# Kernel optimization log

Measured on AMD Instinct MI355X. Metric: run time of the kernel, lower is better.

The kernel has to match this reference:

```python
import jax, jax.numpy as jnp
import numpy as np

WEIGHT_BITS = 4           # weight_bit_width for both convs
SCALE_MIN = 2e-16         # scaling_min_val from CommonIntWeightPerTensorQuant


def fake_quant_per_channel(w, bits):
    """Brevitas-style per-output-channel symmetric narrow-range int fake quant.
    scale = max|w| over each output channel / (2^(bits-1) - 1), STE round."""
    qmax = float(2 ** (bits - 1) - 1)
    absmax = jnp.max(jnp.abs(w.reshape(w.shape[0], -1)), axis=1)
    scale = jnp.maximum(absmax / qmax, SCALE_MIN)
    scale = scale.reshape((-1,) + (1,) * (w.ndim - 1))
    q = jnp.clip(jnp.round(w / scale), -qmax, qmax) * scale
    # straight-through estimator (matches brevitas round_ste)
    return w + jax.lax.stop_gradient(q - w)


def setup_inputs() -> dict:
    key = jax.random.key(0)
    k1, k2, k3, k4 = jax.random.split(key, 4)
    x = jax.random.normal(k1, (32, 384, 56, 56), dtype=jnp.float32)
    # depthwise weight: (out=C, in/groups=1, kH, kW)
    dw_w = jax.random.normal(k2, (384, 1, 3, 3), dtype=jnp.float32) * 0.1
    # pointwise weight: (out, in, 1, 1); pw conv has default bias=True
    pw_w = jax.random.normal(k3, (384, 384, 1, 1), dtype=jnp.float32) * 0.05
    pw_b = jax.random.normal(k4, (384,), dtype=jnp.float32) * 0.01
    return {"x": x, "dw_w": dw_w, "pw_w": pw_w, "pw_b": pw_b}


def reference(x, dw_w, pw_w, pw_b):
    C = dw_w.shape[0]
    dw_q = fake_quant_per_channel(dw_w, WEIGHT_BITS)
    pw_q = fake_quant_per_channel(pw_w, WEIGHT_BITS)
    # depthwise 3x3, stride 1, pad 1
    y = jax.lax.conv_general_dilated(
        x, dw_q, window_strides=(1, 1), padding=((1, 1), (1, 1)),
        dimension_numbers=("NCHW", "OIHW", "NCHW"), feature_group_count=C)
    # pointwise 1x1 + bias
    z = jax.lax.conv_general_dilated(
        y, pw_q, window_strides=(1, 1), padding="VALID",
        dimension_numbers=("NCHW", "OIHW", "NCHW"))
    return z + pw_b[None, :, None, None]
```

## Files before the change

kernel.cpp:

```cpp
#include <hip/hip_runtime.h>
#include <hip/hip_bf16.h>

#define CCH 384
#define HW2 3136
#define HH 56
#define WW 56
#define QMAX 7.0f
#define SCALE_MIN 2e-16f
#define PB 49
#define YSLAB 512
#define YPB 24576
#define ROWP 60
#define CHW 964

typedef _Float16 half8 __attribute__((ext_vector_type(8)));
typedef float f32x4 __attribute__((ext_vector_type(4)));

#define GLOAD_LDS16(g, l) __builtin_amdgcn_global_load_lds( \
    (const __attribute__((address_space(1))) void*)(g), \
    (__attribute__((address_space(3))) void*)(l), 16, 0, 0)


__global__ void quant_dw(const float* __restrict__ dw, float* __restrict__ dwq) {
    int c = blockIdx.x * blockDim.x + threadIdx.x;
    if (c >= CCH) return;
    float w[9];
    float amax = 0.f;
    #pragma unroll
    for (int j = 0; j < 9; ++j) {
        w[j] = dw[c * 9 + j];
        amax = fmaxf(amax, fabsf(w[j]));
    }
    float scale = fmaxf(amax / QMAX, SCALE_MIN);
    #pragma unroll
    for (int j = 0; j < 9; ++j) {
        float q = rintf(w[j] / scale);
        q = fminf(fmaxf(q, -QMAX), QMAX);
        dwq[c * 9 + j] = q * scale;
    }
}

__global__ void quant_pw(const float* __restrict__ pw, _Float16* __restrict__ wpk) {
    int co = blockIdx.x;
    int lane = threadIdx.x;
    float w[6];
    float amax = 0.f;
    #pragma unroll
    for (int j = 0; j < 6; ++j) {
        w[j] = pw[co * CCH + lane + j * 64];
        amax = fmaxf(amax, fabsf(w[j]));
    }
    #pragma unroll
    for (int off = 32; off >= 1; off >>= 1)
        amax = fmaxf(amax, __shfl_xor(amax, off));
    float scale = fmaxf(amax / QMAX, SCALE_MIN);
    #pragma unroll
    for (int j = 0; j < 6; ++j) {
        int ci = lane + j * 64;
        float q = rintf(w[j] / scale);
        q = fminf(fmaxf(q, -QMAX), QMAX);
        float v = q * scale;
        int kk  = ci >> 5;
        int cis = ci & 31;
        int l   = (co & 15) | ((cis >> 3) << 4);
        int idx = (kk * 24 + (co >> 4)) * 512 + l * 8 + (cis & 7);
        wpk[idx] = (_Float16)v;
    }
}


__global__ __launch_bounds__(128) void dw_kernel(
    const float* __restrict__ x, const float* __restrict__ dwq,
    _Float16* __restrict__ ypk)
{
    __shared__ __align__(16) float xs[8 * CHW];

    int bid = blockIdx.x;
    int wg = (bid & 7) * 768 + (bid >> 3);
    int rg = wg & 3;
    int t2 = wg >> 2;
    int c8 = t2 % 48, n = t2 / 48;
    const int h0 = rg * 14;
    const int tid = threadIdx.x;

    const float* xpl = x + ((size_t)n * CCH + (size_t)c8 * 8) * HW2;

    {
        int s = tid >> 3, ch = tid & 7;
        *(f32x4*)&xs[ch * CHW + 4 + s * ROWP + 56] = (f32x4){0.f, 0.f, 0.f, 0.f};
        if (tid < 32) xs[(tid >> 2) * CHW + (tid & 3)] = 0.f;
    }

    {
        const int ch = tid >> 4, idx16 = tid & 15;
        const float* src = xpl + (size_t)ch * HW2;
        #pragma unroll
        for (int j = 0; j < 14; ++j) {
            const int g = j * 16 + idx16;
            const int s = g / 14, q = g - s * 14;
            const int srow = h0 - 1 + s;
            const int crow = srow < 0 ? 0 : (srow > 55 ? 55 : srow);
            f32x4 v = *(const f32x4*)(src + crow * WW + q * 4);
            if (srow != crow) v = (f32x4){0.f, 0.f, 0.f, 0.f};
            *(f32x4*)&xs[ch * CHW + 4 + s * ROWP + q * 4] = v;
        }
    }
    __syncthreads();

    if (tid >= 98) return;

    const int row  = tid / 7;
    const int wseg = tid - row * 7;
    const int w0   = wseg * 8;
    const int qlo  = (w0 - 1) >> 2;

    half8 pk[8];
    #pragma unroll
    for (int ch = 0; ch < 8; ++ch) {
        const float* wq = dwq + (size_t)(c8 * 8 + ch) * 9;
        float wv[9];
        #pragma unroll
        for (int k = 0; k < 9; ++k) wv[k] = wq[k];

        float a[8] = {0.f,0.f,0.f,0.f,0.f,0.f,0.f,0.f};
        #pragma unroll
        for (int dr = 0; dr < 3; ++dr) {
            const int base = ch * CHW + 4 + (row + dr) * ROWP + qlo * 4;
            f32x4 q0 = *(const f32x4*)&xs[base];
            f32x4 q1 = *(const f32x4*)&xs[base + 4];
            f32x4 q2 = *(const f32x4*)&xs[base + 8];
            f32x4 q3 = *(const f32x4*)&xs[base + 12];
            float win[16] = {q0.x,q0.y,q0.z,q0.w, q1.x,q1.y,q1.z,q1.w,
                             q2.x,q2.y,q2.z,q2.w, q3.x,q3.y,q3.z,q3.w};
            #pragma unroll
            for (int j0 = 0; j0 < 8; ++j0) {
                float s0 = a[j0];
                s0 = fmaf(win[3 + j0], wv[dr * 3 + 0], s0);
                s0 = fmaf(win[4 + j0], wv[dr * 3 + 1], s0);
                s0 = fmaf(win[5 + j0], wv[dr * 3 + 2], s0);
                a[j0] = s0;
            }
        }
        #pragma unroll
        for (int j0 = 0; j0 < 8; ++j0) pk[j0][ch] = (_Float16)a[j0];
    }

    const int posb = (h0 + row) * WW + w0;
    _Float16* yn = ypk + (size_t)n * PB * YPB + (size_t)c8 * YSLAB;
    #pragma unroll
    for (int j0 = 0; j0 < 8; ++j0) {
        const int pos = posb + j0;
        *(half8*)(yn + (size_t)(pos >> 6) * YPB + (pos & 63) * 8) = pk[j0];
    }
}


__global__ __launch_bounds__(256) void pw_kernel(
    const _Float16* __restrict__ ypk, const _Float16* __restrict__ wpk,
    const float* __restrict__ bias, float* __restrict__ out)
{
    __shared__ __align__(16) _Float16 ysh[YPB];

    int bid = blockIdx.x;
    int wg = (bid & 7) * 196 + (bid >> 3);
    int n = wg / PB, pb = wg % PB;

    const int t = threadIdx.x;
    const int lane = t & 63;
    const int g = __builtin_amdgcn_readfirstlane(t >> 6);

    const _Float16* yg = ypk + (size_t)(n * PB + pb) * YPB;
    #pragma unroll
    for (int j = 0; j < 12; ++j) {
        GLOAD_LDS16(yg + (j * 256 + t) * 8,
                    ysh + (size_t)(j * 256 + (t & 192)) * 8);
    }
    __syncthreads();

    const int lco = lane & 15;
    const int lkg = lane >> 4;
    const int cbf = g * 6;

    f32x4 acc[6][4];
    #pragma unroll
    for (int mc = 0; mc < 6; ++mc)
        #pragma unroll
        for (int np = 0; np < 4; ++np)
            acc[mc][np] = (f32x4){0.f, 0.f, 0.f, 0.f};

    for (int kk = 0; kk < 12; ++kk) {
        half8 wf[6];
        #pragma unroll
        for (int mc = 0; mc < 6; ++mc)
            wf[mc] = *(const half8*)(wpk + (size_t)(kk * 24 + cbf + mc) * 512 + lane * 8);
        half8 yf[4];
        #pragma unroll
        for (int np = 0; np < 4; ++np)
            yf[np] = *(const half8*)(ysh + kk * 2048 + lkg * 512 + (np * 16 + lco) * 8);
        #pragma unroll
        for (int mc = 0; mc < 6; ++mc)
            #pragma unroll
            for (int np = 0; np < 4; ++np)
                acc[mc][np] = __builtin_amdgcn_mfma_f32_16x16x32_f16(
                    wf[mc], yf[np], acc[mc][np], 0, 0, 0);
    }

    float* ob = out + (size_t)n * CCH * HW2 + (size_t)pb * 64;
    #pragma unroll
    for (int mc = 0; mc < 6; ++mc) {
        #pragma unroll
        for (int r = 0; r < 4; ++r) {
            const int co = g * 96 + mc * 16 + lkg * 4 + r;
            const float bv = bias[co];
            #pragma unroll
            for (int np = 0; np < 4; ++np)
                ob[(size_t)co * HW2 + np * 16 + lco] = acc[mc][np][r] + bv;
        }
    }
}


extern "C" void kernel_launch(void* const* d_in, const int* in_sizes, int n_in,
                              void* d_out, int out_size, void* d_ws, size_t ws_size,
                              hipStream_t stream) {
    const float* x  = (const float*)d_in[0];
    const float* dw = (const float*)d_in[1];
    const float* pw = (const float*)d_in[2];
    const float* pb = (const float*)d_in[3];
    float* out = (float*)d_out;

    float*    dwq = (float*)d_ws;
    _Float16* wpk = (_Float16*)(dwq + CCH * 9);
    _Float16* ypk = wpk + (size_t)CCH * CCH;

    quant_dw<<<2, 256, 0, stream>>>(dw, dwq);
    quant_pw<<<CCH, 64, 0, stream>>>(pw, wpk);

    dw_kernel<<<6144, 128, 0, stream>>>(x, dwq, ypk);
    pw_kernel<<<1568, 256, 0, stream>>>(ypk, wpk, pb, out);
}
```

Measured before the change: 126.0 us.

## Stage depthwise input via direct global-to-LDS loads and vectorize pointwise stores

The depthwise kernel now fills its padded shared-memory tile with global_load_lds DMA instructions instead of register round-trips. Padding and out-of-range slots are served from a zero page that quant_dw writes into the workspace, and the per-channel stride grows to 1024 floats. In the pointwise kernel the MFMA operands are swapped so each lane holds four consecutive output positions, which allows 16-byte vector stores and one bias load per channel block instead of scalar stores. The costs are a larger LDS footprint per block and more complex address arithmetic for the zero-page redirection.

After: 149.5 us. 1.19x slower.

```diff
diff --git a/kernel.cpp b/kernel.cpp
--- a/kernel.cpp
+++ b/kernel.cpp
@@ -11,7 +11,7 @@
 #define YSLAB 512
 #define YPB 24576
 #define ROWP 60
-#define CHW 964
+#define CHF 1024
 
 typedef _Float16 half8 __attribute__((ext_vector_type(8)));
 typedef float f32x4 __attribute__((ext_vector_type(4)));
@@ -21,8 +21,13 @@
     (__attribute__((address_space(3))) void*)(l), 16, 0, 0)
 
 
-__global__ void quant_dw(const float* __restrict__ dw, float* __restrict__ dwq) {
-    int c = blockIdx.x * blockDim.x + threadIdx.x;
+__global__ void quant_dw(const float* __restrict__ dw, float* __restrict__ dwq,
+                         float* __restrict__ zpg) {
+    int tid = threadIdx.x;
+    if (blockIdx.x == 0)
+        *(f32x4*)&zpg[tid * 4] = (f32x4){0.f, 0.f, 0.f, 0.f};
+
+    int c = blockIdx.x * blockDim.x + tid;
     if (c >= CCH) return;
     float w[9];
     float amax = 0.f;
@@ -71,9 +76,9 @@
 
 __global__ __launch_bounds__(128) void dw_kernel(
     const float* __restrict__ x, const float* __restrict__ dwq,
-    _Float16* __restrict__ ypk)
+    const float* __restrict__ zpg, _Float16* __restrict__ ypk)
 {
-    __shared__ __align__(16) float xs[8 * CHW];
+    __shared__ __align__(16) float xs[8 * CHF];
 
     int bid = blockIdx.x;
     int wg = (bid & 7) * 768 + (bid >> 3);
@@ -85,25 +90,19 @@
 
     const float* xpl = x + ((size_t)n * CCH + (size_t)c8 * 8) * HW2;
 
-    {
-        int s = tid >> 3, ch = tid & 7;
-        *(f32x4*)&xs[ch * CHW + 4 + s * ROWP + 56] = (f32x4){0.f, 0.f, 0.f, 0.f};
-        if (tid < 32) xs[(tid >> 2) * CHW + (tid & 3)] = 0.f;
-    }
-
-    {
-        const int ch = tid >> 4, idx16 = tid & 15;
-        const float* src = xpl + (size_t)ch * HW2;
-        #pragma unroll
-        for (int j = 0; j < 14; ++j) {
-            const int g = j * 16 + idx16;
-            const int s = g / 14, q = g - s * 14;
-            const int srow = h0 - 1 + s;
-            const int crow = srow < 0 ? 0 : (srow > 55 ? 55 : srow);
-            f32x4 v = *(const f32x4*)(src + crow * WW + q * 4);
-            if (srow != crow) v = (f32x4){0.f, 0.f, 0.f, 0.f};
-            *(f32x4*)&xs[ch * CHW + 4 + s * ROWP + q * 4] = v;
-        }
+    #pragma unroll
+    for (int j = 0; j < 16; ++j) {
+        const int ch = j >> 1;
+        const unsigned u = (j & 1) * 128 + tid;
+        const unsigned t = u - 1;
+        const unsigned r = t / 15u;
+        const unsigned q = t - r * 15u;
+        const int srow = h0 - 1 + (int)r;
+        const bool zero = (u == 0u) | (u > 240u) | (q == 14u) |
+                          ((unsigned)srow > 55u);
+        const float* src = zero ? (zpg + (tid & 63) * 4)
+                                : (xpl + (size_t)ch * HW2 + srow * WW + q * 4);
+        GLOAD_LDS16(src, xs + (j * 128 + (tid & 64)) * 4);
     }
     __syncthreads();
 
@@ -125,7 +124,7 @@
         float a[8] = {0.f,0.f,0.f,0.f,0.f,0.f,0.f,0.f};
         #pragma unroll
         for (int dr = 0; dr < 3; ++dr) {
-            const int base = ch * CHW + 4 + (row + dr) * ROWP + qlo * 4;
+            const int base = ch * CHF + 4 + (row + dr) * ROWP + qlo * 4;
             f32x4 q0 = *(const f32x4*)&xs[base];
             f32x4 q1 = *(const f32x4*)&xs[base + 4];
             f32x4 q2 = *(const f32x4*)&xs[base + 8];
@@ -202,19 +201,20 @@
             #pragma unroll
             for (int np = 0; np < 4; ++np)
                 acc[mc][np] = __builtin_amdgcn_mfma_f32_16x16x32_f16(
-                    wf[mc], yf[np], acc[mc][np], 0, 0, 0);
-    }
-
-    float* ob = out + (size_t)n * CCH * HW2 + (size_t)pb * 64;
+                    yf[np], wf[mc], acc[mc][np], 0, 0, 0);
+    }
+
     #pragma unroll
     for (int mc = 0; mc < 6; ++mc) {
-        #pragma unroll
-        for (int r = 0; r < 4; ++r) {
-            const int co = g * 96 + mc * 16 + lkg * 4 + r;
-            const float bv = bias[co];
-            #pragma unroll
-            for (int np = 0; np < 4; ++np)
-                ob[(size_t)co * HW2 + np * 16 + lco] = acc[mc][np][r] + bv;
+        const int co = g * 96 + mc * 16 + lco;
+        const float bv = bias[co];
+        float* orow = out + (size_t)n * CCH * HW2 + (size_t)co * HW2
+                          + (size_t)pb * 64 + lkg * 4;
+        #pragma unroll
+        for (int np = 0; np < 4; ++np) {
+            f32x4 v = acc[mc][np];
+            v.x += bv; v.y += bv; v.z += bv; v.w += bv;
+            *(f32x4*)(orow + np * 16) = v;
         }
     }
 }
@@ -230,12 +230,13 @@
     float* out = (float*)d_out;
 
     float*    dwq = (float*)d_ws;
-    _Float16* wpk = (_Float16*)(dwq + CCH * 9);
+    float*    zpg = dwq + CCH * 9;
+    _Float16* wpk = (_Float16*)(zpg + 1024);
     _Float16* ypk = wpk + (size_t)CCH * CCH;
 
-    quant_dw<<<2, 256, 0, stream>>>(dw, dwq);
+    quant_dw<<<2, 256, 0, stream>>>(dw, dwq, zpg);
     quant_pw<<<CCH, 64, 0, stream>>>(pw, wpk);
 
-    dw_kernel<<<6144, 128, 0, stream>>>(x, dwq, ypk);
+    dw_kernel<<<6144, 128, 0, stream>>>(x, dwq, zpg, ypk);
     pw_kernel<<<1568, 256, 0, stream>>>(ypk, wpk, pb, out);
 }
```
